# Optimization experiments

Hardware: AMD Instinct MI355X
Metric: run time of the kernel (lower is better)

Reference implementation:

```python
import jax, jax.numpy as jnp
import numpy as np

N_NODES = 100000


def setup_inputs() -> dict:
    key = jax.random.key(0)
    k1, k2, k3, k4, k5, k6 = jax.random.split(key, 6)
    N, E, DIN, DOUT = N_NODES, 1600000, 64, 64
    feature = jax.random.normal(k1, (N, DIN), dtype=jnp.float32)
    norm = jax.random.uniform(k2, (N, 1), dtype=jnp.float32)  # per-node 1/sqrt(deg)-style norm
    src = jax.random.randint(k3, (E,), 0, N, dtype=jnp.int32)
    dst = jax.random.randint(k4, (E,), 0, N, dtype=jnp.int32)
    W = jax.random.normal(k5, (DOUT, DIN), dtype=jnp.float32) / jnp.sqrt(jnp.float32(DIN))
    b = jax.random.normal(k6, (DOUT,), dtype=jnp.float32)
    return {"feature": feature, "norm": norm, "src": src, "dst": dst, "W": W, "b": b}


def reference(feature, norm, src, dst, W, b):
    # message: h_src * norm_src, gathered per edge -> [E, DIN]
    msg = (feature * norm)[src]
    # reduce: scatter-sum over destination nodes, then renormalize by dst norm
    accum = jax.ops.segment_sum(msg, dst, num_segments=N_NODES) * norm  # [N, DIN]
    # final Linear: accum @ W^T + b
    return accum @ W.T + b
```

## Files before the change

### kernel.cpp

```cpp
#include <hip/hip_runtime.h>
#include <hip/hip_bf16.h>

#define N_NODES 100000
#define D 64
#define BNODES 128
#define NBKT 782
#define SCAP 16
#define BCAP 4608
#define CAP 48
#define SENT 0xFFFFFFFFu

__global__ __launch_bounds__(256) void pre_linear_kernel(
    const float* __restrict__ feature,
    const float* __restrict__ norm,
    const float* __restrict__ W,
    __hip_bfloat16* __restrict__ Zb)
{
    __shared__ float Wt[D * 65];
    __shared__ float accsm[4][D];

    for (int i = threadIdx.x; i < D * D; i += blockDim.x) {
        int o = i >> 6, k = i & 63;
        Wt[k * 65 + o] = W[o * D + k];
    }
    __syncthreads();

    const int lane = threadIdx.x & 63;
    const int wid  = threadIdx.x >> 6;

    float wreg[D];
    #pragma unroll
    for (int k = 0; k < D; ++k) wreg[k] = Wt[k * 65 + lane];
    float* const mysm = &accsm[wid][0];

    const int wave   = (blockIdx.x * blockDim.x + threadIdx.x) >> 6;
    const int nwaves = gridDim.x * (blockDim.x >> 6);

    for (int node = wave; node < N_NODES; node += nwaves) {
        float x = feature[node * D + lane] * norm[node];
        mysm[lane] = x;
        __builtin_amdgcn_wave_barrier();
        float r = 0.f;
        #pragma unroll
        for (int j = 0; j < D / 4; ++j) {
            float4 a4 = *(const float4*)&mysm[j * 4];
            r = fmaf(a4.x, wreg[4 * j + 0], r);
            r = fmaf(a4.y, wreg[4 * j + 1], r);
            r = fmaf(a4.z, wreg[4 * j + 2], r);
            r = fmaf(a4.w, wreg[4 * j + 3], r);
        }
        Zb[node * D + lane] = __float2bfloat16(r);
        __builtin_amdgcn_wave_barrier();
    }
}

__global__ __launch_bounds__(1024) void bin_scatter_kernel(
    const int* __restrict__ src, const int* __restrict__ dst,
    int* __restrict__ bkt_cnt,
    unsigned int* __restrict__ barr,
    int E)
{
    __shared__ unsigned int stage[NBKT][SCAP];
    __shared__ int scnt[NBKT];

    for (int i = threadIdx.x; i < NBKT; i += blockDim.x) scnt[i] = 0;
    __syncthreads();

    const int nthreads = gridDim.x * blockDim.x;
    for (int e = blockIdx.x * blockDim.x + threadIdx.x; e < E; e += nthreads) {
        int t = dst[e];
        int b = t >> 7;
        unsigned u = ((unsigned)src[e] << 7) | (unsigned)(t & 127);
        int slot = atomicAdd(&scnt[b], 1);
        if (slot < SCAP) {
            stage[b][slot] = u;
        } else {
            int g = atomicAdd(&bkt_cnt[b], 16);
            if (g + 16 <= BCAP) {
                unsigned int* dp = barr + (size_t)b * BCAP + g;
                dp[0] = u;
                #pragma unroll
                for (int k = 1; k < 16; ++k) dp[k] = SENT;
            }
        }
    }
    __syncthreads();

    for (int bb = threadIdx.x; bb < NBKT; bb += blockDim.x) {
        int n_live = scnt[bb];
        if (n_live > SCAP) n_live = SCAP;
        if (n_live > 0) {
            int g = atomicAdd(&bkt_cnt[bb], 16);
            if (g + 16 <= BCAP) {
                unsigned int* dp = barr + (size_t)bb * BCAP + g;
                for (int k = 0; k < n_live; ++k) dp[k] = stage[bb][k];
                for (int k = n_live; k < 16; ++k) dp[k] = SENT;
            }
        }
    }
}

__device__ inline float2 bf2f(unsigned int z) {
    float2 r;
    r.x = __uint_as_float(z << 16);
    r.y = __uint_as_float(z & 0xffff0000u);
    return r;
}

__global__ __launch_bounds__(512) void csr_gather_kernel(
    const __hip_bfloat16* __restrict__ Zb,
    const float* __restrict__ norm,
    const int* __restrict__ bkt_cnt,
    const unsigned int* __restrict__ barr,
    const float* __restrict__ bias,
    float* __restrict__ out)
{
    __shared__ int slab[BNODES * CAP];
    __shared__ int lcnt[BNODES];

    const int b   = blockIdx.x;
    const int tid = threadIdx.x;

    for (int i = tid; i < BNODES; i += blockDim.x) lcnt[i] = 0;
    __syncthreads();

    int n = bkt_cnt[b];
    if (n > BCAP) n = BCAP;
    const unsigned int* bp = barr + (size_t)b * BCAP;
    for (int i = tid; i < n; i += blockDim.x) {
        unsigned u = bp[i];
        if (u != SENT) {
            int local = (int)(u & 127);
            int pos = atomicAdd(&lcnt[local], 1);
            if (pos < CAP) slab[local * CAP + pos] = (int)(u >> 7);
        }
    }
    __syncthreads();

    const int lane = tid & 63;
    const int wid  = tid >> 6;
    const int half = lane >> 5;
    const int col  = lane & 31;

    const float bx = bias[2 * col + 0];
    const float by = bias[2 * col + 1];

    for (int nl = wid; nl < BNODES; nl += 8) {
        int node = (b << 7) + nl;
        if (node >= N_NODES) continue;

        int len = lcnt[nl];
        if (len > CAP) len = CAP;
        const int* sl = &slab[nl * CAP];

        float ax = 0.f, ay = 0.f;
        int i = 0;
        for (; i + 8 <= len; i += 8) {
            int s0 = sl[i + 0 + half];
            int s1 = sl[i + 2 + half];
            int s2 = sl[i + 4 + half];
            int s3 = sl[i + 6 + half];
            unsigned z0 = *(const unsigned*)&Zb[s0 * D + 2 * col];
            unsigned z1 = *(const unsigned*)&Zb[s1 * D + 2 * col];
            unsigned z2 = *(const unsigned*)&Zb[s2 * D + 2 * col];
            unsigned z3 = *(const unsigned*)&Zb[s3 * D + 2 * col];
            float2 v0 = bf2f(z0), v1 = bf2f(z1), v2 = bf2f(z2), v3 = bf2f(z3);
            ax += v0.x + v1.x + v2.x + v3.x;
            ay += v0.y + v1.y + v2.y + v3.y;
        }
        for (; i < len; i += 2) {
            int idx = i + half;
            if (idx < len) {
                int s = sl[idx];
                float2 v = bf2f(*(const unsigned*)&Zb[s * D + 2 * col]);
                ax += v.x;
                ay += v.y;
            }
        }

        ax += __shfl(ax, lane ^ 32, 64);
        ay += __shfl(ay, lane ^ 32, 64);

        if (half == 0) {
            float nv = norm[node];
            float2 o;
            o.x = fmaf(nv, ax, bx);
            o.y = fmaf(nv, ay, by);
            *(float2*)&out[node * D + 2 * col] = o;
        }
    }
}

extern "C" void kernel_launch(void* const* d_in, const int* in_sizes, int n_in,
                              void* d_out, int out_size, void* d_ws, size_t ws_size,
                              hipStream_t stream)
{
    const float* feature = (const float*)d_in[0];
    const float* norm    = (const float*)d_in[1];
    const int*   src     = (const int*)d_in[2];
    const int*   dst     = (const int*)d_in[3];
    const float* W       = (const float*)d_in[4];
    const float* b       = (const float*)d_in[5];
    float*       out     = (float*)d_out;

    const int E = in_sizes[2];

    char* p = (char*)d_ws;
    __hip_bfloat16* Zb      = (__hip_bfloat16*)p;  p += (size_t)N_NODES * D * 2;
    unsigned int*   barr    = (unsigned int*)p;    p += (size_t)NBKT * BCAP * 4;
    int*            bkt_cnt = (int*)p;

    hipMemsetAsync(bkt_cnt, 0, (size_t)NBKT * sizeof(int), stream);

    pre_linear_kernel<<<3125, 256, 0, stream>>>(feature, norm, W, Zb);

    bin_scatter_kernel<<<256, 1024, 0, stream>>>(src, dst, bkt_cnt, barr, E);

    csr_gather_kernel<<<NBKT, 512, 0, stream>>>(Zb, norm, bkt_cnt, barr, b, out);
}
```

Baseline: 176.6 us.

## Fold bucket-count reset into pre-linear kernel and widen gather loads

Drops the separate memset by having the pre-linear kernel zero the bucket counters. The gather kernel now reads bucket entries as uint4 and gathers each neighbor row with 8-byte loads across 16 lanes, so one wave covers four edges per instruction instead of two. The partial sums are then reduced with two shuffle stages before a float4 store. This cuts launch overhead and the number of gather load instructions, but leaves fewer lanes per row and adds some shuffle work.

```diff
diff --git a/kernel.cpp b/kernel.cpp
--- a/kernel.cpp
+++ b/kernel.cpp
@@ -14,10 +14,14 @@
     const float* __restrict__ feature,
     const float* __restrict__ norm,
     const float* __restrict__ W,
-    __hip_bfloat16* __restrict__ Zb)
+    __hip_bfloat16* __restrict__ Zb,
+    int* __restrict__ bkt_cnt)
 {
     __shared__ float Wt[D * 65];
     __shared__ float accsm[4][D];
+
+    int gid = blockIdx.x * blockDim.x + threadIdx.x;
+    if (gid < NBKT) bkt_cnt[gid] = 0;
 
     for (int i = threadIdx.x; i < D * D; i += blockDim.x) {
         int o = i >> 6, k = i & 63;
@@ -33,7 +37,7 @@
     for (int k = 0; k < D; ++k) wreg[k] = Wt[k * 65 + lane];
     float* const mysm = &accsm[wid][0];
 
-    const int wave   = (blockIdx.x * blockDim.x + threadIdx.x) >> 6;
+    const int wave   = gid >> 6;
     const int nwaves = gridDim.x * (blockDim.x >> 6);
 
     for (int node = wave; node < N_NODES; node += nwaves) {
@@ -127,23 +131,27 @@
     int n = bkt_cnt[b];
     if (n > BCAP) n = BCAP;
     const unsigned int* bp = barr + (size_t)b * BCAP;
-    for (int i = tid; i < n; i += blockDim.x) {
-        unsigned u = bp[i];
-        if (u != SENT) {
-            int local = (int)(u & 127);
-            int pos = atomicAdd(&lcnt[local], 1);
-            if (pos < CAP) slab[local * CAP + pos] = (int)(u >> 7);
+    for (int i = tid * 4; i < n; i += blockDim.x * 4) {
+        uint4 u4 = *(const uint4*)&bp[i];
+        unsigned us[4] = {u4.x, u4.y, u4.z, u4.w};
+        #pragma unroll
+        for (int j = 0; j < 4; ++j) {
+            unsigned u = us[j];
+            if (u != SENT) {
+                int local = (int)(u & 127);
+                int pos = atomicAdd(&lcnt[local], 1);
+                if (pos < CAP) slab[local * CAP + pos] = (int)(u >> 7);
+            }
         }
     }
     __syncthreads();
 
     const int lane = tid & 63;
     const int wid  = tid >> 6;
-    const int half = lane >> 5;
-    const int col  = lane & 31;
-
-    const float bx = bias[2 * col + 0];
-    const float by = bias[2 * col + 1];
+    const int q    = lane >> 4;
+    const int c    = lane & 15;
+
+    const float4 bi = *(const float4*)&bias[4 * c];
 
     for (int nl = wid; nl < BNODES; nl += 8) {
         int node = (b << 7) + nl;
@@ -153,40 +161,53 @@
         if (len > CAP) len = CAP;
         const int* sl = &slab[nl * CAP];
 
-        float ax = 0.f, ay = 0.f;
+        float ax = 0.f, ay = 0.f, az = 0.f, aw = 0.f;
         int i = 0;
-        for (; i + 8 <= len; i += 8) {
-            int s0 = sl[i + 0 + half];
-            int s1 = sl[i + 2 + half];
-            int s2 = sl[i + 4 + half];
-            int s3 = sl[i + 6 + half];
-            unsigned z0 = *(const unsigned*)&Zb[s0 * D + 2 * col];
-            unsigned z1 = *(const unsigned*)&Zb[s1 * D + 2 * col];
-            unsigned z2 = *(const unsigned*)&Zb[s2 * D + 2 * col];
-            unsigned z3 = *(const unsigned*)&Zb[s3 * D + 2 * col];
-            float2 v0 = bf2f(z0), v1 = bf2f(z1), v2 = bf2f(z2), v3 = bf2f(z3);
-            ax += v0.x + v1.x + v2.x + v3.x;
-            ay += v0.y + v1.y + v2.y + v3.y;
-        }
-        for (; i < len; i += 2) {
-            int idx = i + half;
+        for (; i + 16 <= len; i += 16) {
+            int s0 = sl[i + 0  + q];
+            int s1 = sl[i + 4  + q];
+            int s2 = sl[i + 8  + q];
+            int s3 = sl[i + 12 + q];
+            uint2 z0 = *(const uint2*)&Zb[s0 * D + 4 * c];
+            uint2 z1 = *(const uint2*)&Zb[s1 * D + 4 * c];
+            uint2 z2 = *(const uint2*)&Zb[s2 * D + 4 * c];
+            uint2 z3 = *(const uint2*)&Zb[s3 * D + 4 * c];
+            float2 a0 = bf2f(z0.x), b0 = bf2f(z0.y);
+            float2 a1 = bf2f(z1.x), b1 = bf2f(z1.y);
+            float2 a2 = bf2f(z2.x), b2 = bf2f(z2.y);
+            float2 a3 = bf2f(z3.x), b3 = bf2f(z3.y);
+            ax += a0.x + a1.x + a2.x + a3.x;
+            ay += a0.y + a1.y + a2.y + a3.y;
+            az += b0.x + b1.x + b2.x + b3.x;
+            aw += b0.y + b1.y + b2.y + b3.y;
+        }
+        for (; i < len; i += 4) {
+            int idx = i + q;
             if (idx < len) {
                 int s = sl[idx];
-                float2 v = bf2f(*(const unsigned*)&Zb[s * D + 2 * col]);
-                ax += v.x;
-                ay += v.y;
-            }
-        }
-
+                uint2 z = *(const uint2*)&Zb[s * D + 4 * c];
+                float2 a = bf2f(z.x), bb2 = bf2f(z.y);
+                ax += a.x; ay += a.y; az += bb2.x; aw += bb2.y;
+            }
+        }
+
+        ax += __shfl(ax, lane ^ 16, 64);
+        ay += __shfl(ay, lane ^ 16, 64);
+        az += __shfl(az, lane ^ 16, 64);
+        aw += __shfl(aw, lane ^ 16, 64);
         ax += __shfl(ax, lane ^ 32, 64);
         ay += __shfl(ay, lane ^ 32, 64);
-
-        if (half == 0) {
+        az += __shfl(az, lane ^ 32, 64);
+        aw += __shfl(aw, lane ^ 32, 64);
+
+        if (q == 0) {
             float nv = norm[node];
-            float2 o;
-            o.x = fmaf(nv, ax, bx);
-            o.y = fmaf(nv, ay, by);
-            *(float2*)&out[node * D + 2 * col] = o;
+            float4 o;
+            o.x = fmaf(nv, ax, bi.x);
+            o.y = fmaf(nv, ay, bi.y);
+            o.z = fmaf(nv, az, bi.z);
+            o.w = fmaf(nv, aw, bi.w);
+            *(float4*)&out[node * D + 4 * c] = o;
         }
     }
 }
@@ -210,9 +231,7 @@
     unsigned int*   barr    = (unsigned int*)p;    p += (size_t)NBKT * BCAP * 4;
     int*            bkt_cnt = (int*)p;
 
-    hipMemsetAsync(bkt_cnt, 0, (size_t)NBKT * sizeof(int), stream);
-
-    pre_linear_kernel<<<3125, 256, 0, stream>>>(feature, norm, W, Zb);
+    pre_linear_kernel<<<3125, 256, 0, stream>>>(feature, norm, W, Zb, bkt_cnt);
 
     bin_scatter_kernel<<<256, 1024, 0, stream>>>(src, dst, bkt_cnt, barr, E);
 
```

After: 170.2 us. -3.6%, faster.
